# Kernel optimization log

Hardware: AMD Instinct MI355X
Metric: run time of the kernel (lower is better)

The kernel has to match this reference:

```python
import jax, jax.numpy as jnp
import numpy as np

B, T, D_IN, D_OUT = 4, 2048, 1024, 1024


def setup_inputs() -> dict:
    key = jax.random.key(0)
    k1, k2, k3, k4 = jax.random.split(key, 4)
    x = jax.random.normal(k1, (B, T, D_IN), dtype=jnp.float32)
    W_q = jax.random.normal(k2, (D_OUT, D_IN), dtype=jnp.float32) * 0.02
    W_k = jax.random.normal(k3, (D_OUT, D_IN), dtype=jnp.float32) * 0.02
    W_v = jax.random.normal(k4, (D_OUT, D_IN), dtype=jnp.float32) * 0.02
    return {"x": x, "W_q": W_q, "W_k": W_k, "W_v": W_v}


def reference(x, W_q, W_k, W_v):
    b, t, d_in = x.shape
    d_out = W_q.shape[0]
    # Linear projections (torch Linear: y = x @ W.T), no bias
    q = jnp.einsum("btd,od->bto", x, W_q)
    k = jnp.einsum("btd,od->bto", x, W_k)
    v = jnp.einsum("btd,od->bto", x, W_v)
    # Raw scores [b, t, t]
    scores = jnp.einsum("bqd,bkd->bqk", q, k)
    # Faithful to the source: tril with diagonal=1 => position i sees j <= i+1
    mask = jnp.tril(jnp.ones((t, t), dtype=bool), k=1)
    scores = jnp.where(mask, scores, -jnp.inf)
    # Scale by sqrt(d_out) (full d_out, single head), stable softmax
    attn = jax.nn.softmax(scores / jnp.sqrt(jnp.asarray(d_out, x.dtype)), axis=-1)
    # dropout=0.0 -> identity
    return jnp.einsum("bqk,bkd->bqd", attn, v)
```

## Files before the change

kernel.cpp:

```cpp
#include <hip/hip_runtime.h>
#include <hip/hip_bf16.h>

typedef unsigned short u16;
typedef __attribute__((ext_vector_type(8))) short short8v;
typedef __attribute__((ext_vector_type(4))) float float4v;

__device__ inline u16 f2b(float f) {
  __hip_bfloat16 h = __float2bfloat16(f);
  union { __hip_bfloat16 h; u16 s; } u;
  u.h = h;
  return u.s;
}

__device__ inline float b2f(u16 s) {
  union { u16 s[2]; float f; } u;
  u.s[0] = 0; u.s[1] = s;
  return u.f;
}

__device__ inline void gload_lds16(const u16* g, u16* l) {
  __builtin_amdgcn_global_load_lds(
      (const __attribute__((address_space(1))) void*)g,
      (__attribute__((address_space(3))) void*)l, 16, 0, 0);
}

__global__ __launch_bounds__(256) void cvt_f32_bf16(const float* __restrict__ in,
                                                    u16* __restrict__ out, int n4) {
  for (int i = blockIdx.x * blockDim.x + threadIdx.x; i < n4;
       i += gridDim.x * blockDim.x) {
    float4 v = ((const float4*)in)[i];
    ushort4 o;
    o.x = f2b(v.x); o.y = f2b(v.y); o.z = f2b(v.z); o.w = f2b(v.w);
    ((ushort4*)out)[i] = o;
  }
}

__global__ __launch_bounds__(256)
void cvt_w3(const float* __restrict__ wa, const float* __restrict__ wb,
            const float* __restrict__ wc, u16* __restrict__ oa,
            u16* __restrict__ ob, u16* __restrict__ oc, int n4each) {
  int i = blockIdx.x * blockDim.x + threadIdx.x;
  const float* src; u16* dst; int off;
  if (i < n4each)            { src = wa; dst = oa; off = i; }
  else if (i < 2 * n4each)   { src = wb; dst = ob; off = i - n4each; }
  else                       { src = wc; dst = oc; off = i - 2 * n4each; }
  float4 v = ((const float4*)src)[off];
  ushort4 o;
  o.x = f2b(v.x); o.y = f2b(v.y); o.z = f2b(v.z); o.w = f2b(v.w);
  ((ushort4*)dst)[off] = o;
}

template <typename CT>
__device__ __forceinline__ void gemm_core(
    const u16* __restrict__ A, int lda,
    const u16* __restrict__ B, int ldb,
    CT* __restrict__ C, int ldc, int m0, int n0, int nk) {
  constexpr int A_U16 = 8192;
  constexpr int TILE_U16 = 16384;
  constexpr int TILE_BYTES = 32768;
  __shared__ __align__(16) u16 lds[2 * TILE_U16];

  const int tid  = threadIdx.x;
  const int lane = tid & 63;
  const int wid  = tid >> 6;
  const int wr   = wid >> 1;
  const int wc   = wid & 1;

  const u16* gsrc[8];
  int loff[8];
#pragma unroll
  for (int j = 0; j < 4; ++j) {
    int c = tid + j * 256;
    int r = c >> 3;
    int kg = ((c & 7) ^ (r & 7)) * 8;
    gsrc[j] = A + (long)(m0 + r) * lda + kg;
    loff[j] = c * 8;
  }
#pragma unroll
  for (int j = 0; j < 4; ++j) {
    int c = tid + j * 256;
    int r = c >> 3;
    int kg = ((c & 7) ^ (r & 7)) * 8;
    gsrc[4 + j] = B + (long)(n0 + r) * ldb + kg;
    loff[4 + j] = A_U16 + c * 8;
  }

#define STAGE_ALL(T_, DST_)                                                 \
  {                                                                         \
    _Pragma("unroll")                                                       \
    for (int s = 0; s < 8; ++s)                                             \
      gload_lds16(gsrc[s] + (long)(T_) * 64, (DST_) + loff[s]);             \
  }

  const int kl  = (lane >> 4) * 16;
  const int swz = (lane & 7) << 4;
  const int kx0 = kl ^ swz;
  const int kx1 = (64 + kl) ^ swz;
  const int abase = (wr * 64 + (lane & 15)) * 128;
  const int bbase = 2 * A_U16 + (wc * 64 + (lane & 15)) * 128;

  float4v acc[4][4];
#pragma unroll
  for (int i = 0; i < 4; ++i)
#pragma unroll
    for (int j = 0; j < 4; ++j)
      acc[i][j] = (float4v){0.f, 0.f, 0.f, 0.f};

  STAGE_ALL(0, lds);
  asm volatile("s_waitcnt vmcnt(0)" ::: "memory");
  __builtin_amdgcn_s_barrier();

  for (int t = 0; t < nk; ++t) {
    const char* bb = (const char*)lds + (t & 1) * TILE_BYTES;
    u16* sb = lds + ((t & 1) ^ 1) * TILE_U16;

    if (t + 1 < nk) STAGE_ALL(t + 1, sb);

    short8v a0[4], b0[4], a1[4], b1[4];
#pragma unroll
    for (int mi = 0; mi < 4; ++mi)
      a0[mi] = *(const short8v*)(bb + abase + mi * 2048 + kx0);
#pragma unroll
    for (int ni = 0; ni < 4; ++ni)
      b0[ni] = *(const short8v*)(bb + bbase + ni * 2048 + kx0);
    __builtin_amdgcn_sched_barrier(0);
#pragma unroll
    for (int mi = 0; mi < 4; ++mi)
      a1[mi] = *(const short8v*)(bb + abase + mi * 2048 + kx1);
#pragma unroll
    for (int ni = 0; ni < 4; ++ni)
      b1[ni] = *(const short8v*)(bb + bbase + ni * 2048 + kx1);

    asm volatile("s_waitcnt lgkmcnt(8)" ::: "memory");
    __builtin_amdgcn_sched_barrier(0);
    __builtin_amdgcn_s_setprio(1);
#pragma unroll
    for (int mi = 0; mi < 4; ++mi)
#pragma unroll
      for (int ni = 0; ni < 4; ++ni)
        acc[mi][ni] = __builtin_amdgcn_mfma_f32_16x16x32_bf16(
            a0[mi], b0[ni], acc[mi][ni], 0, 0, 0);
    __builtin_amdgcn_s_setprio(0);

    asm volatile("s_waitcnt lgkmcnt(0)" ::: "memory");
    __builtin_amdgcn_sched_barrier(0);
    __builtin_amdgcn_s_setprio(1);
#pragma unroll
    for (int mi = 0; mi < 4; ++mi)
#pragma unroll
      for (int ni = 0; ni < 4; ++ni)
        acc[mi][ni] = __builtin_amdgcn_mfma_f32_16x16x32_bf16(
            a1[mi], b1[ni], acc[mi][ni], 0, 0, 0);
    __builtin_amdgcn_s_setprio(0);

    asm volatile("s_waitcnt vmcnt(0)" ::: "memory");
    __builtin_amdgcn_s_barrier();
  }
#undef STAGE_ALL

  const int r0base = m0 + wr * 64 + ((lane >> 4) << 2);
  const int cbase  = n0 + wc * 64 + (lane & 15);
#pragma unroll
  for (int mi = 0; mi < 4; ++mi) {
#pragma unroll
    for (int ni = 0; ni < 4; ++ni) {
      const int r0 = r0base + mi * 16;
      const int cc = cbase + ni * 16;
#pragma unroll
      for (int r = 0; r < 4; ++r) {
        float v = acc[mi][ni][r];
        if constexpr (__is_same(CT, float)) C[(long)(r0 + r) * ldc + cc] = v;
        else                                C[(long)(r0 + r) * ldc + cc] = f2b(v);
      }
    }
  }
}

template <int MODE, typename CT>
__global__ __launch_bounds__(256, 2)
void gemm8(const u16* __restrict__ A, int lda, long sA,
           const u16* __restrict__ B, int ldb, long sB,
           CT* __restrict__ C, int ldc, long sC, int K) {
  const int z = blockIdx.z;
  int bx = blockIdx.x;
  if (MODE == 2 && z < 2) bx = gridDim.x - 1 - bx;
  const int m0 = bx * 128;
  const int n0 = blockIdx.y * 128;
  int Keff = K;
  if (MODE == 2) Keff = min(m0 + 129, K);
  gemm_core<CT>(A + (long)z * sA, lda, B + (long)z * sB, ldb,
                C + (long)z * sC, ldc, m0, n0, (Keff + 63) >> 6);
}

__global__ __launch_bounds__(256, 2)
void gemm_vts(const u16* __restrict__ xb, const u16* __restrict__ wv,
              const u16* __restrict__ qk, u16* __restrict__ vt,
              u16* __restrict__ S) {
  const int bid = blockIdx.x;
  const u16 *A, *B; u16* C; int lda, ldc, m0, n0;
  if (bid < 512) {
    A = wv; B = xb; C = vt; lda = 1024; ldc = 8192;
    m0 = (bid & 7) * 128; n0 = (bid >> 3) * 128;
  } else {
    const int sid = bid - 512;
    const int z = sid >> 8, r = sid & 255;
    m0 = (r & 15) * 128; n0 = (r >> 4) * 128;
    if (n0 > m0 + 128) return;
    const long zo = (long)z * 4194304;
    A = qk + zo; B = qk + zo + 1024; C = S + zo;
    lda = 2048; ldc = 2048;
  }
  gemm_core<u16>(A, lda, B, lda, C, ldc, m0, n0, 16);
}

__global__ __launch_bounds__(256)
void softmax_kernel(u16* __restrict__ SP, int T) {
  const int  i    = blockIdx.x & (T - 1);
  const long base = (long)blockIdx.x * T;
  const int  nvis = min(i + 2, T);
  const int  capJ = min(T, ((i >> 7) << 7) + 192);
  const float scale = 0.03125f;

  __shared__ float red[4];

  const int j0 = threadIdx.x * 8;
  float v[8];
  float m = -INFINITY;
  if (j0 < nvis) {
    short8v raw = *(const short8v*)&SP[base + j0];
#pragma unroll
    for (int e = 0; e < 8; ++e) {
      float f = (j0 + e < nvis) ? b2f((u16)raw[e]) * scale : -INFINITY;
      v[e] = f;
      m = fmaxf(m, f);
    }
  }
#pragma unroll
  for (int o = 32; o; o >>= 1) m = fmaxf(m, __shfl_xor(m, o));
  const int wid = threadIdx.x >> 6;
  if ((threadIdx.x & 63) == 0) red[wid] = m;
  __syncthreads();
  m = fmaxf(fmaxf(red[0], red[1]), fmaxf(red[2], red[3]));
  __syncthreads();

  float s = 0.f;
  if (j0 < nvis) {
#pragma unroll
    for (int e = 0; e < 8; ++e) {
      float p = (j0 + e < nvis) ? __expf(v[e] - m) : 0.f;
      v[e] = p;
      s += p;
    }
  }
#pragma unroll
  for (int o = 32; o; o >>= 1) s += __shfl_xor(s, o);
  if ((threadIdx.x & 63) == 0) red[wid] = s;
  __syncthreads();
  s = red[0] + red[1] + red[2] + red[3];
  const float inv = 1.0f / s;

  if (j0 < capJ) {
    short8v o8;
#pragma unroll
    for (int e = 0; e < 8; ++e)
      o8[e] = (short)f2b((j0 + e < nvis) ? v[e] * inv : 0.f);
    *(short8v*)&SP[base + j0] = o8;
  }
}

extern "C" void kernel_launch(void* const* d_in, const int* in_sizes, int n_in,
                              void* d_out, int out_size, void* d_ws, size_t ws_size,
                              hipStream_t stream) {
  const float* x  = (const float*)d_in[0];
  const float* Wq = (const float*)d_in[1];
  const float* Wk = (const float*)d_in[2];
  const float* Wv = (const float*)d_in[3];
  float* out = (float*)d_out;

  const int B = 4, T = 2048, D = 1024;
  const int M = B * T;
  const long TT = (long)T * T;

  char* ws = (char*)d_ws;
  u16* qk  = (u16*)(ws);
  u16* vt  = (u16*)(ws + (32l << 20));
  u16* xb  = (u16*)(ws + (48l << 20));
  u16* wqk = (u16*)(ws + (64l << 20));
  u16* wv  = (u16*)(ws + (68l << 20));
  u16* S   = (u16*)(ws + (72l << 20));

  cvt_f32_bf16<<<2048, 256, 0, stream>>>(x, xb, (M * D) / 4);
  cvt_w3<<<3 * (D * D / 4) / 256, 256, 0, stream>>>(
      Wq, Wk, Wv, wqk, wqk + (long)D * D, wv, D * D / 4);

  gemm8<0, u16><<<dim3(M / 128, 2 * D / 128, 1), 256, 0, stream>>>(
      xb, D, 0, wqk, D, 0, qk, 2 * D, 0, D);

  gemm_vts<<<512 + 1024, 256, 0, stream>>>(xb, wv, qk, vt, S);

  softmax_kernel<<<B * T, 256, 0, stream>>>(S, T);

  gemm8<2, float><<<dim3(T / 128, D / 128, B), 256, 0, stream>>>(
      S, T, TT,
      vt, M, T,
      out, D, (long)T * D, T);
}
```

Measured before the change: 152.9 us.

## Split-K causal PV GEMM with atomic accumulation and compact causal S grid

The PV GEMM is rewritten as a split-K kernel. Each causal row tile's K range is cut into chunks of up to 8 k-tiles, and partial results are accumulated into a zeroed fp32 output with atomic adds, which balances the triangular workload across more blocks. The QK^T part of gemm_vts now launches only the causal lower-triangular tiles through a prefix-sum lookup, so no launched blocks exit early. This adds a memset and atomic traffic on the output, and makes the fp32 summation order nondeterministic.

```diff
diff --git a/kernel.cpp b/kernel.cpp
--- a/kernel.cpp
+++ b/kernel.cpp
@@ -50,7 +50,7 @@
   ((ushort4*)dst)[off] = o;
 }
 
-template <typename CT>
+template <typename CT, bool ACCUM>
 __device__ __forceinline__ void gemm_core(
     const u16* __restrict__ A, int lda,
     const u16* __restrict__ B, int ldb,
@@ -169,27 +169,23 @@
 #pragma unroll
       for (int r = 0; r < 4; ++r) {
         float v = acc[mi][ni][r];
-        if constexpr (__is_same(CT, float)) C[(long)(r0 + r) * ldc + cc] = v;
-        else                                C[(long)(r0 + r) * ldc + cc] = f2b(v);
+        if constexpr (ACCUM)
+          unsafeAtomicAdd(&C[(long)(r0 + r) * ldc + cc], v);
+        else if constexpr (__is_same(CT, float))
+          C[(long)(r0 + r) * ldc + cc] = v;
+        else
+          C[(long)(r0 + r) * ldc + cc] = f2b(v);
       }
     }
   }
 }
 
-template <int MODE, typename CT>
 __global__ __launch_bounds__(256, 2)
-void gemm8(const u16* __restrict__ A, int lda, long sA,
-           const u16* __restrict__ B, int ldb, long sB,
-           CT* __restrict__ C, int ldc, long sC, int K) {
-  const int z = blockIdx.z;
-  int bx = blockIdx.x;
-  if (MODE == 2 && z < 2) bx = gridDim.x - 1 - bx;
-  const int m0 = bx * 128;
-  const int n0 = blockIdx.y * 128;
-  int Keff = K;
-  if (MODE == 2) Keff = min(m0 + 129, K);
-  gemm_core<CT>(A + (long)z * sA, lda, B + (long)z * sB, ldb,
-                C + (long)z * sC, ldc, m0, n0, (Keff + 63) >> 6);
+void gemm_qk(const u16* __restrict__ A, int lda,
+             const u16* __restrict__ B, int ldb,
+             u16* __restrict__ C, int ldc, int K) {
+  gemm_core<u16, false>(A, lda, B, ldb, C, ldc,
+                        blockIdx.x * 128, blockIdx.y * 128, K >> 6);
 }
 
 __global__ __launch_bounds__(256, 2)
@@ -197,20 +193,43 @@
               const u16* __restrict__ qk, u16* __restrict__ vt,
               u16* __restrict__ S) {
   const int bid = blockIdx.x;
-  const u16 *A, *B; u16* C; int lda, ldc, m0, n0;
   if (bid < 512) {
-    A = wv; B = xb; C = vt; lda = 1024; ldc = 8192;
-    m0 = (bid & 7) * 128; n0 = (bid >> 3) * 128;
+    gemm_core<u16, false>(wv, 1024, xb, 1024, vt, 8192,
+                          (bid & 7) * 128, (bid >> 3) * 128, 16);
   } else {
+    const int cum2[16] = {2, 5, 9, 14, 20, 27, 35, 44,
+                          54, 65, 77, 90, 104, 119, 135, 151};
     const int sid = bid - 512;
-    const int z = sid >> 8, r = sid & 255;
-    m0 = (r & 15) * 128; n0 = (r >> 4) * 128;
-    if (n0 > m0 + 128) return;
+    const int z = sid / 151, r = sid % 151;
+    int x = 0;
+    while (r >= cum2[x]) ++x;
+    const int y = r - (x ? cum2[x - 1] : 0);
     const long zo = (long)z * 4194304;
-    A = qk + zo; B = qk + zo + 1024; C = S + zo;
-    lda = 2048; ldc = 2048;
-  }
-  gemm_core<u16>(A, lda, B, lda, C, ldc, m0, n0, 16);
+    gemm_core<u16, false>(qk + zo, 2048, qk + zo + 1024, 2048, S + zo, 2048,
+                          x * 128, y * 128, 16);
+  }
+}
+
+__global__ __launch_bounds__(256, 2)
+void gemm_pv(const u16* __restrict__ S, const u16* __restrict__ vt,
+             float* __restrict__ out) {
+  const int cum[16] = {1, 2, 3, 5, 7, 9, 11, 14,
+                       17, 20, 23, 27, 31, 35, 39, 43};
+  const int bid = blockIdx.x;
+  const int z = bid / 344, r = bid % 344;
+  const int y = r / 43;
+  const int c = 42 - (r % 43);
+  int x = 0;
+  while (c >= cum[x]) ++x;
+  const int ci = c - (x ? cum[x - 1] : 0);
+  const int nk = (x == 15) ? 32 : (2 * x + 3);
+  const int k0t = ci * 8;
+  const int nkc = min(nk - k0t, 8);
+  const long k0e = (long)k0t * 64;
+  gemm_core<float, true>(S + (long)z * 4194304 + k0e, 2048,
+                         vt + (long)z * 2048 + k0e, 8192,
+                         out + (long)z * 2097152, 1024,
+                         x * 128, y * 128, nkc);
 }
 
 __global__ __launch_bounds__(256)
@@ -279,7 +298,6 @@
 
   const int B = 4, T = 2048, D = 1024;
   const int M = B * T;
-  const long TT = (long)T * T;
 
   char* ws = (char*)d_ws;
   u16* qk  = (u16*)(ws);
@@ -289,19 +307,18 @@
   u16* wv  = (u16*)(ws + (68l << 20));
   u16* S   = (u16*)(ws + (72l << 20));
 
+  hipMemsetAsync(out, 0, (size_t)out_size * sizeof(float), stream);
+
   cvt_f32_bf16<<<2048, 256, 0, stream>>>(x, xb, (M * D) / 4);
   cvt_w3<<<3 * (D * D / 4) / 256, 256, 0, stream>>>(
       Wq, Wk, Wv, wqk, wqk + (long)D * D, wv, D * D / 4);
 
-  gemm8<0, u16><<<dim3(M / 128, 2 * D / 128, 1), 256, 0, stream>>>(
-      xb, D, 0, wqk, D, 0, qk, 2 * D, 0, D);
-
-  gemm_vts<<<512 + 1024, 256, 0, stream>>>(xb, wv, qk, vt, S);
+  gemm_qk<<<dim3(M / 128, 2 * D / 128), 256, 0, stream>>>(
+      xb, D, wqk, D, qk, 2 * D, D);
+
+  gemm_vts<<<512 + 604, 256, 0, stream>>>(xb, wv, qk, vt, S);
 
   softmax_kernel<<<B * T, 256, 0, stream>>>(S, T);
 
-  gemm8<2, float><<<dim3(T / 128, D / 128, B), 256, 0, stream>>>(
-      S, T, TT,
-      vt, M, T,
-      out, D, (long)T * D, T);
-}
+  gemm_pv<<<1376, 256, 0, stream>>>(S, vt, out);
+}
```

Measured after the change: 213.3 us. 1.39x slower.

## Launch only lower-triangular score tiles and patch boundary entries in softmax

Applied to the files above, without the earlier changes.

The QK^T score GEMM now launches only the 136 lower-triangular 128x128 tiles per batch instead of launching 256 and early-exiting. The tile grid is now strictly diagonal-inclusive, so the single super-diagonal element at block boundaries (j=i+1 across a tile edge) is no longer computed. Softmax recomputes that element as a direct q·k dot product for boundary rows. The two conversion kernels are merged into one launch and the GEMM wrappers are specialised. This removes idle blocks and one launch, at the cost of extra per-row work and a branch in softmax.

```diff
diff --git a/kernel.cpp b/kernel.cpp
--- a/kernel.cpp
+++ b/kernel.cpp
@@ -3,6 +3,7 @@
 
 typedef unsigned short u16;
 typedef __attribute__((ext_vector_type(8))) short short8v;
+typedef __attribute__((ext_vector_type(4))) short short4v;
 typedef __attribute__((ext_vector_type(4))) float float4v;
 
 __device__ inline u16 f2b(float f) {
@@ -24,30 +25,28 @@
       (__attribute__((address_space(3))) void*)l, 16, 0, 0);
 }
 
-__global__ __launch_bounds__(256) void cvt_f32_bf16(const float* __restrict__ in,
-                                                    u16* __restrict__ out, int n4) {
-  for (int i = blockIdx.x * blockDim.x + threadIdx.x; i < n4;
+__global__ __launch_bounds__(256)
+void cvt_all(const float* __restrict__ x, const float* __restrict__ Wq,
+             const float* __restrict__ Wk, const float* __restrict__ Wv,
+             u16* __restrict__ xb, u16* __restrict__ wqk, u16* __restrict__ wv,
+             int nx, int nw) {
+  const int ntot = nx + 3 * nw;
+  for (int i = blockIdx.x * blockDim.x + threadIdx.x; i < ntot;
        i += gridDim.x * blockDim.x) {
-    float4 v = ((const float4*)in)[i];
+    const float* src; u16* dst; int off;
+    if (i < nx) { src = x; dst = xb; off = i; }
+    else {
+      int wi = i - nx;
+      int w = wi / nw;
+      off = wi - w * nw;
+      src = (w == 0) ? Wq : (w == 1) ? Wk : Wv;
+      dst = (w == 0) ? wqk : (w == 1) ? wqk + 4l * nw : wv;
+    }
+    float4 v = ((const float4*)src)[off];
     ushort4 o;
     o.x = f2b(v.x); o.y = f2b(v.y); o.z = f2b(v.z); o.w = f2b(v.w);
-    ((ushort4*)out)[i] = o;
-  }
-}
-
-__global__ __launch_bounds__(256)
-void cvt_w3(const float* __restrict__ wa, const float* __restrict__ wb,
-            const float* __restrict__ wc, u16* __restrict__ oa,
-            u16* __restrict__ ob, u16* __restrict__ oc, int n4each) {
-  int i = blockIdx.x * blockDim.x + threadIdx.x;
-  const float* src; u16* dst; int off;
-  if (i < n4each)            { src = wa; dst = oa; off = i; }
-  else if (i < 2 * n4each)   { src = wb; dst = ob; off = i - n4each; }
-  else                       { src = wc; dst = oc; off = i - 2 * n4each; }
-  float4 v = ((const float4*)src)[off];
-  ushort4 o;
-  o.x = f2b(v.x); o.y = f2b(v.y); o.z = f2b(v.z); o.w = f2b(v.w);
-  ((ushort4*)dst)[off] = o;
+    ((ushort4*)dst)[off] = o;
+  }
 }
 
 template <typename CT>
@@ -176,20 +175,12 @@
   }
 }
 
-template <int MODE, typename CT>
 __global__ __launch_bounds__(256, 2)
-void gemm8(const u16* __restrict__ A, int lda, long sA,
-           const u16* __restrict__ B, int ldb, long sB,
-           CT* __restrict__ C, int ldc, long sC, int K) {
-  const int z = blockIdx.z;
-  int bx = blockIdx.x;
-  if (MODE == 2 && z < 2) bx = gridDim.x - 1 - bx;
-  const int m0 = bx * 128;
-  const int n0 = blockIdx.y * 128;
-  int Keff = K;
-  if (MODE == 2) Keff = min(m0 + 129, K);
-  gemm_core<CT>(A + (long)z * sA, lda, B + (long)z * sB, ldb,
-                C + (long)z * sC, ldc, m0, n0, (Keff + 63) >> 6);
+void gemm_qk(const u16* __restrict__ A, int lda,
+             const u16* __restrict__ B, int ldb,
+             u16* __restrict__ C, int ldc, int K) {
+  gemm_core<u16>(A, lda, B, ldb, C, ldc,
+                 blockIdx.x * 128, blockIdx.y * 128, K >> 6);
 }
 
 __global__ __launch_bounds__(256, 2)
@@ -197,31 +188,53 @@
               const u16* __restrict__ qk, u16* __restrict__ vt,
               u16* __restrict__ S) {
   const int bid = blockIdx.x;
-  const u16 *A, *B; u16* C; int lda, ldc, m0, n0;
   if (bid < 512) {
-    A = wv; B = xb; C = vt; lda = 1024; ldc = 8192;
-    m0 = (bid & 7) * 128; n0 = (bid >> 3) * 128;
+    gemm_core<u16>(wv, 1024, xb, 1024, vt, 8192,
+                   (bid & 7) * 128, (bid >> 3) * 128, 16);
   } else {
+    const int cum[16] = {1, 3, 6, 10, 15, 21, 28, 36,
+                         45, 55, 66, 78, 91, 105, 120, 136};
     const int sid = bid - 512;
-    const int z = sid >> 8, r = sid & 255;
-    m0 = (r & 15) * 128; n0 = (r >> 4) * 128;
-    if (n0 > m0 + 128) return;
+    const int z = sid / 136, r = sid % 136;
+    int x = 0;
+    while (r >= cum[x]) ++x;
+    const int y = r - (x ? cum[x - 1] : 0);
     const long zo = (long)z * 4194304;
-    A = qk + zo; B = qk + zo + 1024; C = S + zo;
-    lda = 2048; ldc = 2048;
-  }
-  gemm_core<u16>(A, lda, B, lda, C, ldc, m0, n0, 16);
+    gemm_core<u16>(qk + zo, 2048, qk + zo + 1024, 2048, S + zo, 2048,
+                   x * 128, y * 128, 16);
+  }
 }
 
 __global__ __launch_bounds__(256)
-void softmax_kernel(u16* __restrict__ SP, int T) {
-  const int  i    = blockIdx.x & (T - 1);
-  const long base = (long)blockIdx.x * T;
+void softmax_kernel(u16* __restrict__ SP, const u16* __restrict__ qk, int T) {
+  const int  iz   = blockIdx.x;
+  const int  i    = iz & (T - 1);
+  const long base = (long)iz * T;
   const int  nvis = min(i + 2, T);
   const int  capJ = min(T, ((i >> 7) << 7) + 192);
   const float scale = 0.03125f;
+  const bool brow = ((i & 127) == 127) && (i < T - 128);
 
   __shared__ float red[4];
+  const int wid = threadIdx.x >> 6;
+
+  float sb = 0.f;
+  if (brow) {
+    const u16* qrow = qk + (long)iz * 2048;
+    const u16* krow = qk + (long)(iz + 1) * 2048 + 1024;
+    const int c = threadIdx.x * 4;
+    short4v qv = *(const short4v*)&qrow[c];
+    short4v kv = *(const short4v*)&krow[c];
+    float p = 0.f;
+#pragma unroll
+    for (int e = 0; e < 4; ++e) p += b2f((u16)qv[e]) * b2f((u16)kv[e]);
+#pragma unroll
+    for (int o = 32; o; o >>= 1) p += __shfl_xor(p, o);
+    if ((threadIdx.x & 63) == 0) red[wid] = p;
+    __syncthreads();
+    sb = red[0] + red[1] + red[2] + red[3];
+    __syncthreads();
+  }
 
   const int j0 = threadIdx.x * 8;
   float v[8];
@@ -229,15 +242,14 @@
   if (j0 < nvis) {
     short8v raw = *(const short8v*)&SP[base + j0];
 #pragma unroll
-    for (int e = 0; e < 8; ++e) {
-      float f = (j0 + e < nvis) ? b2f((u16)raw[e]) * scale : -INFINITY;
-      v[e] = f;
-      m = fmaxf(m, f);
-    }
+    for (int e = 0; e < 8; ++e)
+      v[e] = (j0 + e < nvis) ? b2f((u16)raw[e]) * scale : -INFINITY;
+    if (brow && j0 == i + 1) v[0] = sb * scale;
+#pragma unroll
+    for (int e = 0; e < 8; ++e) m = fmaxf(m, v[e]);
   }
 #pragma unroll
   for (int o = 32; o; o >>= 1) m = fmaxf(m, __shfl_xor(m, o));
-  const int wid = threadIdx.x >> 6;
   if ((threadIdx.x & 63) == 0) red[wid] = m;
   __syncthreads();
   m = fmaxf(fmaxf(red[0], red[1]), fmaxf(red[2], red[3]));
@@ -266,6 +278,21 @@
       o8[e] = (short)f2b((j0 + e < nvis) ? v[e] * inv : 0.f);
     *(short8v*)&SP[base + j0] = o8;
   }
+}
+
+__global__ __launch_bounds__(256, 2)
+void gemm_pv(const u16* __restrict__ S, const u16* __restrict__ vt,
+             float* __restrict__ out, int K) {
+  const int z = blockIdx.z;
+  int bx = blockIdx.x;
+  if (z < 2) bx = gridDim.x - 1 - bx;
+  const int m0 = bx * 128;
+  const int n0 = blockIdx.y * 128;
+  const int Keff = min(m0 + 129, K);
+  gemm_core<float>(S + (long)z * 4194304, 2048,
+                   vt + (long)z * 2048, 8192,
+                   out + (long)z * 2097152, 1024,
+                   m0, n0, (Keff + 63) >> 6);
 }
 
 extern "C" void kernel_launch(void* const* d_in, const int* in_sizes, int n_in,
@@ -279,7 +306,6 @@
 
   const int B = 4, T = 2048, D = 1024;
   const int M = B * T;
-  const long TT = (long)T * T;
 
   char* ws = (char*)d_ws;
   u16* qk  = (u16*)(ws);
@@ -289,19 +315,15 @@
   u16* wv  = (u16*)(ws + (68l << 20));
   u16* S   = (u16*)(ws + (72l << 20));
 
-  cvt_f32_bf16<<<2048, 256, 0, stream>>>(x, xb, (M * D) / 4);
-  cvt_w3<<<3 * (D * D / 4) / 256, 256, 0, stream>>>(
-      Wq, Wk, Wv, wqk, wqk + (long)D * D, wv, D * D / 4);
-
-  gemm8<0, u16><<<dim3(M / 128, 2 * D / 128, 1), 256, 0, stream>>>(
-      xb, D, 0, wqk, D, 0, qk, 2 * D, 0, D);
-
-  gemm_vts<<<512 + 1024, 256, 0, stream>>>(xb, wv, qk, vt, S);
-
-  softmax_kernel<<<B * T, 256, 0, stream>>>(S, T);
-
-  gemm8<2, float><<<dim3(T / 128, D / 128, B), 256, 0, stream>>>(
-      S, T, TT,
-      vt, M, T,
-      out, D, (long)T * D, T);
-}
+  cvt_all<<<2048, 256, 0, stream>>>(x, Wq, Wk, Wv, xb, wqk, wv,
+                                    (M * D) / 4, (D * D) / 4);
+
+  gemm_qk<<<dim3(M / 128, 2 * D / 128), 256, 0, stream>>>(
+      xb, D, wqk, D, qk, 2 * D, D);
+
+  gemm_vts<<<512 + 544, 256, 0, stream>>>(xb, wv, qk, vt, S);
+
+  softmax_kernel<<<B * T, 256, 0, stream>>>(S, qk, T);
+
+  gemm_pv<<<dim3(T / 128, D / 128, B), 256, 0, stream>>>(S, vt, out, T);
+}
```

Measured after the change: 158.0 us. +3.3%, slower.
